# Optimization experiments

Hardware: AMD Instinct MI355X
Metric: run time of the kernel (lower is better)

## Reference

```python
import jax, jax.numpy as jnp
import numpy as np

B = 262144
D = 128          # d_model
DFF = 4 * D      # 512, FFN expansion
T = 16           # num_tiles
TPC = 4          # tiles_per_cluster
NC = T // TPC    # 4 clusters
NOPS = 8         # len(OPCODES)
EMB = 32
FEAT = EMB + 17  # 49
TW, SW, DW = 0.01, 0.005, 0.01  # ternary / sparsity / diversity weights


def ternary_quant(W):
    # per-tile ternary quantization: threshold at 0.7 * mean|W|, scale = mean|W|
    s0 = jnp.mean(jnp.abs(W))
    return s0 * jnp.sign(W) * (jnp.abs(W) > 0.7 * s0).astype(W.dtype)


def setup_inputs() -> dict:
    key = jax.random.key(0)
    ks = jax.random.split(key, 16)
    inp = {
        'op_idx': jax.random.randint(ks[0], (B,), 0, NOPS),
        'a': jax.random.randint(ks[1], (B,), 0, 256),
        'b': jax.random.randint(ks[2], (B,), 0, 256),
        'c': jax.random.randint(ks[3], (B,), 0, 2),
        # parameters
        'op_embed': jax.random.normal(ks[4], (NOPS, EMB), jnp.float32),
        'W_in': jax.random.normal(ks[5], (FEAT, D), jnp.float32) / np.sqrt(FEAT),
        'b_in': jnp.zeros((D,), jnp.float32),
        'Wr': jax.random.normal(ks[6], (D, T), jnp.float32) / np.sqrt(D),
        'W1': jax.random.normal(ks[7], (T, D, DFF), jnp.float32) / np.sqrt(D),
        'W2': jax.random.normal(ks[8], (T, DFF, D), jnp.float32) / np.sqrt(DFF),
        'Wh1': jax.random.normal(ks[9], (D, 64), jnp.float32) / np.sqrt(D),
        'bh1': jnp.zeros((64,), jnp.float32),
        'Wh2': jax.random.normal(ks[10], (64, 8), jnp.float32) / np.sqrt(64),
        'bh2': jnp.zeros((8,), jnp.float32),
    }
    return inp


def reference(op_embed, W_in, b_in, Wr, W1, W2, Wh1, bh1, Wh2, bh2, op_idx, a, b, c):
    bits = lambda v: ((v[:, None] >> jnp.arange(8)) & 1).astype(jnp.float32)  # [B,8]
    emb = op_embed[op_idx]  # [B,32]
    x = jnp.concatenate([emb, bits(a), bits(b), c[:, None].astype(jnp.float32)], axis=1)  # [B,49]
    x = x @ W_in + b_in  # [B,D]

    # tile routing (top-1)
    logits = x @ Wr                      # [B,T]
    probs = jax.nn.softmax(logits, -1)
    idx = jnp.argmax(probs, -1)          # [B]
    gate = jnp.max(probs, -1)            # [B]

    # ternary-quantized per-tile FFN weights
    W1q = jax.vmap(ternary_quant)(W1)    # [T,D,DFF]
    W2q = jax.vmap(ternary_quant)(W2)    # [T,DFF,D]

    out = jnp.zeros_like(x)
    for t in range(T):  # fixed small tile set
        y = jax.nn.gelu(x @ W1q[t]) @ W2q[t]          # [B,D]
        out = out + jnp.where((idx == t)[:, None], y, 0.0)
    out = out * gate[:, None]

    # aux losses
    one_hot = jax.nn.one_hot(idx, T, dtype=x.dtype)
    frac = one_hot.mean(0)               # tokens per tile
    meanp = probs.mean(0)                # mean router prob per tile
    sparsity = T * jnp.sum(frac * meanp)              # load-balance (Switch-style)
    tern = jnp.mean(jnp.abs(W1 - W1q)) + jnp.mean(jnp.abs(W2 - W2q))
    cp = meanp.reshape(NC, TPC).sum(-1)               # cluster usage
    diversity = jnp.sum(cp * jnp.log(cp + 1e-9))      # negative entropy
    aux = TW * tern + SW * sparsity + DW * diversity

    h = jax.nn.relu(out @ Wh1 + bh1)
    result = jax.nn.sigmoid(h @ Wh2 + bh2)  # [B,8]
    return result, idx, aux
```

## Files before the change

### kernel.cpp

```cpp
#include <hip/hip_runtime.h>
#include <hip/hip_bf16.h>
#include <math.h>

typedef __attribute__((ext_vector_type(8))) short short8;
typedef __attribute__((ext_vector_type(4))) float floatx4;
typedef __attribute__((ext_vector_type(4))) unsigned int uintx4;
typedef __attribute__((ext_vector_type(2))) unsigned int uintx2;

__device__ __forceinline__ unsigned short f2bf(float f) {
    unsigned int u = __float_as_uint(f);
    unsigned int r = (u + 0x7fffu + ((u >> 16) & 1u)) >> 16;
    return (unsigned short)r;
}

__device__ __forceinline__ unsigned int cvtpk(float a, float b) {
    unsigned int r;
    asm("v_cvt_pk_bf16_f32 %0, %1, %2" : "=v"(r) : "v"(a), "v"(b));
    return r;
}

__device__ __forceinline__ void permlane32_swap(unsigned int &a, unsigned int &b) {
    asm volatile("v_permlane32_swap_b32 %0, %1" : "+v"(a), "+v"(b));
}
__device__ __forceinline__ void permlane16_swap(unsigned int &a, unsigned int &b) {
    asm volatile("v_permlane16_swap_b32 %0, %1" : "+v"(a), "+v"(b));
}

__device__ __forceinline__ float gelu_f(float u) {
    float u2 = u * u;
    float p = __builtin_fmaf(u2, -0.102943242f, -2.302208184f);
    float z = p * u;
    float e;
    asm("v_exp_f32 %0, %1" : "=v"(e) : "v"(z));
    return u * __builtin_amdgcn_rcpf(1.0f + e);
}

__device__ __forceinline__ floatx4 mfma16(short8 a, short8 b, floatx4 c) {
    return __builtin_amdgcn_mfma_f32_16x16x32_bf16(a, b, c, 0, 0, 0);
}


__global__ __launch_bounds__(256) void k_prep1(
        const float* __restrict__ W1, const float* __restrict__ W2,
        float* __restrict__ partials,
        const float* __restrict__ op_embed, const float* __restrict__ W_in,
        const float* __restrict__ b_in,
        float* embW, float* Ta, float* Tb, float* Tc) {
    __shared__ float red[256];
    int bid = blockIdx.x;
    if (bid < 512) {
        bool isW1 = bid < 256;
        const float* W = (isW1 ? W1 : W2) + (long)(isW1 ? bid : bid - 256) * 4096;
        float s = 0.f;
        #pragma unroll
        for (int i = 0; i < 4; i++) {
            floatx4 v = *(const floatx4*)(W + i * 1024 + threadIdx.x * 4);
            s += fabsf(v[0]) + fabsf(v[1]) + fabsf(v[2]) + fabsf(v[3]);
        }
        red[threadIdx.x] = s; __syncthreads();
        for (int st = 128; st > 0; st >>= 1) {
            if (threadIdx.x < st) red[threadIdx.x] += red[threadIdx.x + st];
            __syncthreads();
        }
        if (threadIdx.x == 0) partials[bid] = red[0];
    } else {
        int i = (bid - 512) * 256 + threadIdx.x;
        if (i < 1024) {
            int op = i >> 7, j = i & 127;
            float s = b_in[j];
            #pragma unroll
            for (int k = 0; k < 32; k++) s += op_embed[op * 32 + k] * W_in[k * 128 + j];
            embW[i] = s;
        } else if (i < 1024 + 32768) {
            int r = i - 1024; int a = r >> 7, j = r & 127;
            float s = 0.f;
            #pragma unroll
            for (int bit = 0; bit < 8; bit++) if ((a >> bit) & 1) s += W_in[(32 + bit) * 128 + j];
            Ta[r] = s;
        } else if (i < 33792 + 32768) {
            int r = i - 33792; int b = r >> 7, j = r & 127;
            float s = 0.f;
            #pragma unroll
            for (int bit = 0; bit < 8; bit++) if ((b >> bit) & 1) s += W_in[(40 + bit) * 128 + j];
            Tb[r] = s;
        } else if (i < 66560 + 128) {
            int j = i - 66560; Tc[j] = W_in[48 * 128 + j];
        }
    }
}


__global__ __launch_bounds__(256) void k_prep2(
        const float* __restrict__ W1, const float* __restrict__ W2,
        const float* __restrict__ partials,
        unsigned short* __restrict__ W1qT, unsigned short* __restrict__ W2qT,
        float* ternsum,
        const float* __restrict__ embW, const float* __restrict__ Ta,
        const float* __restrict__ Tb, const float* __restrict__ Tc,
        const float* __restrict__ Wr,
        float* embWr, float* TaR, float* TbR, float* TcR) {
    __shared__ unsigned short Lq[4096];
    __shared__ float red[256];
    int blk = blockIdx.x;
    if (blk >= 512) {
        int i = (blk - 512) * 256 + threadIdx.x;
        int row = i >> 4, t = i & 15;
        const float* src; float* dst;
        if (row < 8)        { src = embW + row * 128;        dst = embWr + i; }
        else if (row < 264) { src = Ta + (row - 8) * 128;    dst = TaR + (row - 8) * 16 + t; }
        else if (row < 520) { src = Tb + (row - 264) * 128;  dst = TbR + (row - 264) * 16 + t; }
        else if (row == 520){ src = Tc;                      dst = TcR + t; }
        else return;
        float s = 0.f;
        for (int j = 0; j < 128; j++) s += src[j] * Wr[j * 16 + t];
        *dst = s;
        return;
    }
    bool isW1 = blk < 256;
    int rb = isW1 ? blk : blk - 256;
    int t = rb >> 4, slab = rb & 15;
    const float* part = partials + (isW1 ? 0 : 256) + t * 16;
    float ssum = 0.f;
    #pragma unroll
    for (int i = 0; i < 16; i++) ssum += part[i];
    float s = ssum * (1.0f / 65536.0f);
    float thr = 0.7f * s;
    unsigned int us = (unsigned int)f2bf(s);
    int tid = threadIdx.x;
    float dsum = 0.f;
    if (isW1) {
        int f0 = slab * 32;
        int d = tid >> 1, fh = (tid & 1) * 16;
        const float* src = W1 + (long)t * 65536 + d * 512 + f0 + fh;
        #pragma unroll
        for (int i = 0; i < 4; i++) {
            floatx4 w = *(const floatx4*)(src + i * 4);
            #pragma unroll
            for (int r = 0; r < 4; r++) {
                float wv = w[r];
                float aw = fabsf(wv);
                bool big = aw > thr;
                dsum += big ? fabsf(aw - s) : aw;
                unsigned int sign15 = (__float_as_uint(wv) >> 16) & 0x8000u;
                unsigned short q = big ? (unsigned short)(us | sign15) : (unsigned short)0;
                Lq[(fh + i * 4 + r) * 128 + d] = q;
            }
        }
    } else {
        int d0 = slab * 8;
        int f = tid * 2;
        const float* src = W2 + (long)t * 65536 + f * 128 + d0;
        #pragma unroll
        for (int rr = 0; rr < 2; rr++) {
            #pragma unroll
            for (int i = 0; i < 2; i++) {
                floatx4 w = *(const floatx4*)(src + rr * 128 + i * 4);
                #pragma unroll
                for (int r = 0; r < 4; r++) {
                    float wv = w[r];
                    float aw = fabsf(wv);
                    bool big = aw > thr;
                    dsum += big ? fabsf(aw - s) : aw;
                    unsigned int sign15 = (__float_as_uint(wv) >> 16) & 0x8000u;
                    unsigned short q = big ? (unsigned short)(us | sign15) : (unsigned short)0;
                    Lq[(i * 4 + r) * 512 + f + rr] = q;
                }
            }
        }
    }
    __syncthreads();
    unsigned short* dst = (isW1 ? W1qT : W2qT) + (long)t * 65536 + slab * 4096;
    const uintx4* Ls = (const uintx4*)Lq;
    uintx4* D4 = (uintx4*)dst;
    D4[tid] = Ls[tid];
    D4[tid + 256] = Ls[tid + 256];
    red[tid] = dsum; __syncthreads();
    for (int st2 = 128; st2 > 0; st2 >>= 1) {
        if (tid < st2) red[tid] += red[tid + st2];
        __syncthreads();
    }
    if (tid == 0) atomicAdd(ternsum, red[0]);
}


__global__ __launch_bounds__(256) void k_main3(
        const int* __restrict__ op_idx, const int* __restrict__ a_in,
        const int* __restrict__ b_in_i, const int* __restrict__ c_in,
        const float* __restrict__ embW, const float* __restrict__ Ta,
        const float* __restrict__ Tb, const float* __restrict__ Tc,
        const float* __restrict__ embWr, const float* __restrict__ TaR,
        const float* __restrict__ TbR, const float* __restrict__ TcR,
        unsigned short* __restrict__ xq, float* __restrict__ gate_out,
        float* psum, int* cnt, float* __restrict__ d_idx,
        const unsigned short* __restrict__ W2qT, const float* __restrict__ Wh1,
        unsigned short* __restrict__ W23qT) {
    __shared__ float sp[4][16];
    __shared__ int sc[4][16];
    __shared__ float wcol[128];

    if (blockIdx.x >= 1024) {
        int b2 = blockIdx.x - 1024;
        int t = b2 >> 6, h = b2 & 63;
        if (threadIdx.x < 128) wcol[threadIdx.x] = Wh1[threadIdx.x * 64 + h];
        __syncthreads();
        int k2 = threadIdx.x * 2;
        const unsigned short* w2 = W2qT + (long)t * 65536 + k2;
        float a0 = 0.f, a1 = 0.f;
        #pragma unroll 8
        for (int d = 0; d < 128; d++) {
            unsigned int u = *(const unsigned int*)(w2 + d * 512);
            float w = wcol[d];
            a0 += w * __uint_as_float(u << 16);
            a1 += w * __uint_as_float(u & 0xffff0000u);
        }
        *(unsigned int*)(W23qT + ((long)(t * 64 + h)) * 512 + k2) = cvtpk(a0, a1);
        return;
    }

    int gid = blockIdx.x * 256 + threadIdx.x;
    int lane = threadIdx.x & 63;
    int j = lane & 15;
    int grpbase = lane & 48;
    float psum_acc = 0.f; int cnt_acc = 0;

    #pragma unroll 1
    for (int it = 0; it < 16; it++) {
        int tok = it * 16384 + (gid >> 4);
        int op = op_idx[tok], a = a_in[tok], b = b_in_i[tok], c = c_in[tok];
        float cf = (float)c;

        float lg = embWr[op * 16 + j] + TaR[a * 16 + j] + TbR[b * 16 + j] + cf * TcR[j];
        float m = lg;
        m = fmaxf(m, __shfl_xor(m, 8, 16));
        m = fmaxf(m, __shfl_xor(m, 4, 16));
        m = fmaxf(m, __shfl_xor(m, 2, 16));
        m = fmaxf(m, __shfl_xor(m, 1, 16));
        float p = __expf(lg - m);
        float s = p;
        s += __shfl_xor(s, 8, 16);
        s += __shfl_xor(s, 4, 16);
        s += __shfl_xor(s, 2, 16);
        s += __shfl_xor(s, 1, 16);
        float g = __builtin_amdgcn_rcpf(s);
        unsigned long long ball = __ballot(lg == m);
        int bi = __ffsll((unsigned long long)((ball >> grpbase) & 0xffffULL)) - 1;
        psum_acc += p * g;
        cnt_acc += (j == bi) ? 1 : 0;
        if (j == 0) { gate_out[tok] = g; d_idx[tok] = (float)bi; }

        int d0 = j * 8;
        const floatx4* E  = (const floatx4*)(embW + op * 128 + d0);
        const floatx4* A4 = (const floatx4*)(Ta + a * 128 + d0);
        const floatx4* B4 = (const floatx4*)(Tb + b * 128 + d0);
        const floatx4* C4 = (const floatx4*)(Tc + d0);
        floatx4 v0 = E[0] + A4[0] + B4[0] + cf * C4[0];
        floatx4 v1 = E[1] + A4[1] + B4[1] + cf * C4[1];
        uintx4 o;
        o[0] = cvtpk(v0[0], v0[1]);
        o[1] = cvtpk(v0[2], v0[3]);
        o[2] = cvtpk(v1[0], v1[1]);
        o[3] = cvtpk(v1[2], v1[3]);
        *(uintx4*)(xq + (long)tok * 128 + d0) = o;
    }

    psum_acc += __shfl_xor(psum_acc, 16);
    psum_acc += __shfl_xor(psum_acc, 32);
    cnt_acc += __shfl_xor(cnt_acc, 16);
    cnt_acc += __shfl_xor(cnt_acc, 32);
    int wv = threadIdx.x >> 6;
    if (lane < 16) { sp[wv][j] = psum_acc; sc[wv][j] = cnt_acc; }
    __syncthreads();
    if (threadIdx.x < 16) {
        int jj = threadIdx.x;
        atomicAdd(&psum[jj], sp[0][jj] + sp[1][jj] + sp[2][jj] + sp[3][jj]);
        atomicAdd(&cnt[jj], sc[0][jj] + sc[1][jj] + sc[2][jj] + sc[3][jj]);
    }
}


__global__ void k_scatter(const float* __restrict__ d_idx, const int* __restrict__ cnt,
                          int* fill, int* __restrict__ bucket) {
    __shared__ int lc[16], lbase[16];
    if (threadIdx.x < 16) lc[threadIdx.x] = 0;
    __syncthreads();
    int offs[16];
    {
        int off = 0;
        #pragma unroll
        for (int tt = 0; tt < 16; tt++) { offs[tt] = off; off += cnt[tt]; }
    }
    int tok = blockIdx.x * 256 + threadIdx.x;
    int t = (int)d_idx[tok];
    int lpos = atomicAdd(&lc[t], 1);
    __syncthreads();
    if (threadIdx.x < 16) lbase[threadIdx.x] = atomicAdd(&fill[threadIdx.x], lc[threadIdx.x]);
    __syncthreads();
    bucket[offs[t] + lbase[t] + lpos] = tok;
}


__global__ __launch_bounds__(256, 3) void k_ffn(
    const unsigned short* __restrict__ xq, const float* __restrict__ gate,
    const int* __restrict__ bucket, const int* __restrict__ cnt_g,
    const float* __restrict__ psum_g, const float* __restrict__ ternsum_g,
    const unsigned short* __restrict__ W1qT, const unsigned short* __restrict__ W23qT,
    const float* __restrict__ Wh2, const float* __restrict__ bh1,
    const float* __restrict__ bh2,
    float* __restrict__ result, float* __restrict__ d_aux) {

    extern __shared__ __align__(16) unsigned char smem[];
    unsigned short* Ax = (unsigned short*)smem;
    float* Red = (float*)(smem + 17408);
    int*   toks = (int*)(smem + 33792);
    float* gats = (float*)(smem + 34048);
    float* Wh2l = (float*)(smem + 34304);
    float* bh2l = (float*)(smem + 36352);
    float* bh1l = (float*)(smem + 36384);

    int bid = blockIdx.x;
    int t = -1, ci = 0, nt = 0, base = 0;
    {
        int coff = 0, off = 0;
        #pragma unroll 1
        for (int tt = 0; tt < 16; tt++) {
            int c = cnt_g[tt];
            int ch = (c + 63) >> 6;
            if (t < 0 && bid < coff + ch) { t = tt; ci = bid - coff; nt = c; base = off + ci * 64; }
            coff += ch; off += c;
        }
    }
    if (t < 0) return;
    int nvalid = nt - ci * 64; if (nvalid > 64) nvalid = 64;

    int tid = threadIdx.x;
    if (tid < 64) {
        int tk = (tid < nvalid) ? bucket[base + tid] : -1;
        toks[tid] = tk;
        gats[tid] = (tk >= 0) ? gate[tk] : 0.0f;
    }
    Wh2l[tid] = Wh2[tid];
    Wh2l[tid + 256] = Wh2[tid + 256];
    if (tid < 8) bh2l[tid] = bh2[tid];
    else if (tid < 72) bh1l[tid - 8] = bh1[tid - 8];
    __syncthreads();

    #pragma unroll
    for (int it = 0; it < 4; it++) {
        int seg = it * 256 + tid; int r = seg >> 4, sg = seg & 15;
        int tk = toks[r];
        uintx4 v = {0u, 0u, 0u, 0u};
        if (tk >= 0) v = *(const uintx4*)(xq + (long)tk * 128 + sg * 8);
        *(uintx4*)(Ax + r * 136 + sg * 8) = v;
    }
    __syncthreads();

    int lane = tid & 63, dh = tid >> 6;
    int lane15 = lane & 15, lgrp = lane >> 4;

    floatx4 acc3[4][4];
    #pragma unroll
    for (int i = 0; i < 4; i++)
        #pragma unroll
        for (int j = 0; j < 4; j++) acc3[i][j] = (floatx4){0.f, 0.f, 0.f, 0.f};

    const unsigned short* w1p  = W1qT + (long)t * 65536 + (dh * 32 + lane15) * 128 + lgrp * 8;
    const unsigned short* w23p = W23qT + (long)t * 32768 + lane15 * 512 + dh * 32 + lgrp * 8;
    int ho0 = dh * 8192;
    int ho1 = ((dh + 1) & 3) * 8192;
    int ho2 = ((dh + 2) & 3) * 8192;
    int ho3 = ((dh + 3) & 3) * 8192;

    for (int nc = 0; nc < 4; nc++) {
        floatx4 acc1[2][4];
        #pragma unroll
        for (int i = 0; i < 2; i++)
            #pragma unroll
            for (int j = 0; j < 4; j++) acc1[i][j] = (floatx4){0.f, 0.f, 0.f, 0.f};

        const unsigned short* w1c = w1p + nc * 16384;
        #pragma unroll
        for (int kk = 0; kk < 4; kk++) {
            short8 af0 = *(const short8*)(w1c + kk * 32);
            short8 af1 = *(const short8*)(w1c + 2048 + kk * 32);
            int ko = kk * 32 + lgrp * 8;
            #pragma unroll
            for (int mt = 0; mt < 4; mt++) {
                short8 bf = *(const short8*)(Ax + (mt * 16 + lane15) * 136 + ko);
                acc1[0][mt] = mfma16(af0, bf, acc1[0][mt]);
                acc1[1][mt] = mfma16(af1, bf, acc1[1][mt]);
            }
        }

        const unsigned short* w23c = w23p + nc * 128;
        short8 af23_0 = *(const short8*)(w23c + ho0);
        short8 af23_1 = *(const short8*)(w23c + ho1);
        short8 af23_2 = *(const short8*)(w23c + ho2);
        short8 af23_3 = *(const short8*)(w23c + ho3);

        #pragma unroll
        for (int mt = 0; mt < 4; mt++) {
            floatx4 v0 = acc1[0][mt], v1 = acc1[1][mt];
            unsigned int X0 = cvtpk(gelu_f(v0[0]), gelu_f(v0[1]));
            unsigned int X1 = cvtpk(gelu_f(v0[2]), gelu_f(v0[3]));
            unsigned int Y0 = cvtpk(gelu_f(v1[0]), gelu_f(v1[1]));
            unsigned int Y1 = cvtpk(gelu_f(v1[2]), gelu_f(v1[3]));
            permlane32_swap(X0, Y0);
            permlane16_swap(X0, Y0);
            permlane32_swap(X1, Y1);
            permlane16_swap(X1, Y1);
            union { uintx4 u; short8 s; } bu;
            bu.u[0] = X0; bu.u[1] = X1; bu.u[2] = Y0; bu.u[3] = Y1;
            short8 bfrag = bu.s;
            acc3[0][mt] = mfma16(af23_0, bfrag, acc3[0][mt]);
            acc3[1][mt] = mfma16(af23_1, bfrag, acc3[1][mt]);
            acc3[2][mt] = mfma16(af23_2, bfrag, acc3[2][mt]);
            acc3[3][mt] = mfma16(af23_3, bfrag, acc3[3][mt]);
        }
    }

    floatx4 fin[4];
    #pragma unroll
    for (int mt = 0; mt < 4; mt++) fin[mt] = acc3[0][mt];
    float* myslot = Red + dh * 1024;
    int lofs = lane * 4;
    #pragma unroll
    for (int mt = 0; mt < 4; mt++)
        *(floatx4*)(myslot + mt * 256 + lofs) = acc3[1][mt];
    __syncthreads();
    {
        const float* ps = Red + ((dh + 3) & 3) * 1024;
        #pragma unroll
        for (int mt = 0; mt < 4; mt++)
            fin[mt] += *(const floatx4*)(ps + mt * 256 + lofs);
    }
    __syncthreads();
    #pragma unroll
    for (int mt = 0; mt < 4; mt++)
        *(floatx4*)(myslot + mt * 256 + lofs) = acc3[2][mt];
    __syncthreads();
    {
        const float* ps = Red + ((dh + 2) & 3) * 1024;
        #pragma unroll
        for (int mt = 0; mt < 4; mt++)
            fin[mt] += *(const floatx4*)(ps + mt * 256 + lofs);
    }
    __syncthreads();
    #pragma unroll
    for (int mt = 0; mt < 4; mt++)
        *(floatx4*)(myslot + mt * 256 + lofs) = acc3[3][mt];
    __syncthreads();
    {
        const float* ps = Red + ((dh + 1) & 3) * 1024;
        #pragma unroll
        for (int mt = 0; mt < 4; mt++)
            fin[mt] += *(const floatx4*)(ps + mt * 256 + lofs);
    }

    float* H = (float*)Ax;
    int hb = dh * 16 + lgrp * 4;
    floatx4 b4 = *(const floatx4*)(bh1l + hb);
    #pragma unroll
    for (int mt = 0; mt < 4; mt++) {
        int m = mt * 16 + lane15;
        float gm = gats[m];
        floatx4 v;
        v[0] = fmaxf(fin[mt][0] * gm + b4[0], 0.f);
        v[1] = fmaxf(fin[mt][1] * gm + b4[1], 0.f);
        v[2] = fmaxf(fin[mt][2] * gm + b4[2], 0.f);
        v[3] = fmaxf(fin[mt][3] * gm + b4[3], 0.f);
        *(floatx4*)(H + m * 68 + hb) = v;
    }
    __syncthreads();

    int mloc = tid >> 2, c0 = (tid & 3) * 2;
    int tk = toks[mloc];
    float z0 = bh2l[c0], z1 = bh2l[c0 + 1];
    const floatx4* Hr4 = (const floatx4*)(H + mloc * 68);
    #pragma unroll
    for (int h4 = 0; h4 < 16; h4++) {
        floatx4 hv = Hr4[h4];
        #pragma unroll
        for (int r = 0; r < 4; r++) {
            int h = h4 * 4 + r;
            z0 += hv[r] * Wh2l[h * 8 + c0];
            z1 += hv[r] * Wh2l[h * 8 + c0 + 1];
        }
    }
    if (tk >= 0) {
        float2 rr;
        rr.x = __builtin_amdgcn_rcpf(1.0f + __expf(-z0));
        rr.y = __builtin_amdgcn_rcpf(1.0f + __expf(-z1));
        *(float2*)(result + (long)tk * 8 + c0) = rr;
    }

    if (bid == 0 && tid == 0) {
        const float Bf = 262144.0f;
        float tern = ternsum_g[0] * (1.0f / 1048576.0f);
        float sp = 0.f; float cp[4] = {0.f, 0.f, 0.f, 0.f};
        for (int tt = 0; tt < 16; tt++) {
            float frac = (float)cnt_g[tt] / Bf, mp = psum_g[tt] / Bf;
            sp += frac * mp; cp[tt >> 2] += mp;
        }
        float dv = 0.f;
        for (int cc = 0; cc < 4; cc++) dv += cp[cc] * logf(cp[cc] + 1e-9f);
        d_aux[0] = 0.01f * tern + 0.005f * (16.0f * sp) + 0.01f * dv;
    }
}


extern "C" void kernel_launch(void* const* d_in, const int* in_sizes, int n_in,
                              void* d_out, int out_size, void* d_ws, size_t ws_size,
                              hipStream_t stream) {
    const int* op_idx = (const int*)d_in[0];
    const int* a_in   = (const int*)d_in[1];
    const int* b_in_i = (const int*)d_in[2];
    const int* c_in   = (const int*)d_in[3];
    const float* op_embed = (const float*)d_in[4];
    const float* W_in  = (const float*)d_in[5];
    const float* b_in  = (const float*)d_in[6];
    const float* Wr    = (const float*)d_in[7];
    const float* W1    = (const float*)d_in[8];
    const float* W2    = (const float*)d_in[9];
    const float* Wh1   = (const float*)d_in[10];
    const float* bh1   = (const float*)d_in[11];
    const float* Wh2   = (const float*)d_in[12];
    const float* bh2   = (const float*)d_in[13];

    const long B = in_sizes[0];
    float* result = (float*)d_out;
    float* d_idx  = (float*)d_out + B * 8;
    float* d_aux  = (float*)d_out + B * 9;

    unsigned char* ws = (unsigned char*)d_ws;
    unsigned short* xq    = (unsigned short*)(ws + 0);
    unsigned short* W1qT  = (unsigned short*)(ws + 67108864);
    unsigned short* W2qT  = (unsigned short*)(ws + 69206016);
    unsigned short* W23qT = (unsigned short*)(ws + 71303168);
    float* gate  = (float*)(ws + 72351744);
    int*   bucket= (int*)  (ws + 73400320);
    float* Ta    = (float*)(ws + 74448896);
    float* Tb    = (float*)(ws + 74579968);
    float* embW  = (float*)(ws + 74711040);
    float* Tc    = (float*)(ws + 74715136);
    float* TaR   = (float*)(ws + 74715648);
    float* TbR   = (float*)(ws + 74732032);
    float* embWr = (float*)(ws + 74748416);
    float* TcR   = (float*)(ws + 74748928);
    float* partials = (float*)(ws + 74748992);
    unsigned char* acc = ws + 74751040;
    float* ternsum = (float*)(acc + 0);
    float* psum    = (float*)(acc + 64);
    int*   cnt     = (int*)(acc + 128);
    int*   fill    = (int*)(acc + 192);

    hipMemsetAsync(acc, 0, 256, stream);

    k_prep1<<<773, 256, 0, stream>>>(W1, W2, partials, op_embed, W_in, b_in,
                                     embW, Ta, Tb, Tc);
    k_prep2<<<545, 256, 0, stream>>>(W1, W2, partials, W1qT, W2qT, ternsum,
                                     embW, Ta, Tb, Tc, Wr, embWr, TaR, TbR, TcR);
    k_main3<<<2048, 256, 0, stream>>>(op_idx, a_in, b_in_i, c_in,
                                      embW, Ta, Tb, Tc, embWr, TaR, TbR, TcR,
                                      xq, gate, psum, cnt, d_idx,
                                      W2qT, Wh1, W23qT);
    k_scatter<<<(int)(B / 256), 256, 0, stream>>>(d_idx, cnt, fill, bucket);
    k_ffn<<<4112, 256, 36640, stream>>>(xq, gate, bucket, cnt, psum, ternsum,
                                        W1qT, W23qT, Wh2, bh1, bh2, result, d_aux);
}
```

Measured before the change: 266.6 us.

## Recompute input embeddings inside FFN kernel instead of materializing xq

Removes the bf16 xq activation buffer written by the routing kernel and read back by the FFN kernel. The FFN kernel now gathers op/a/b/c per token and rebuilds each row from the small precomputed embedding tables. This drops roughly 64MB of write plus read traffic in exchange for extra table gathers and index loads inside the FFN kernel. It also reorders the first GEMM loop so all W1 fragments are loaded up front and the nc loop is fully unrolled, which raises register pressure.

```diff
diff --git a/kernel.cpp b/kernel.cpp
--- a/kernel.cpp
+++ b/kernel.cpp
@@ -5,7 +5,6 @@
 typedef __attribute__((ext_vector_type(8))) short short8;
 typedef __attribute__((ext_vector_type(4))) float floatx4;
 typedef __attribute__((ext_vector_type(4))) unsigned int uintx4;
-typedef __attribute__((ext_vector_type(2))) unsigned int uintx2;
 
 __device__ __forceinline__ unsigned short f2bf(float f) {
     unsigned int u = __float_as_uint(f);
@@ -186,11 +185,9 @@
 __global__ __launch_bounds__(256) void k_main3(
         const int* __restrict__ op_idx, const int* __restrict__ a_in,
         const int* __restrict__ b_in_i, const int* __restrict__ c_in,
-        const float* __restrict__ embW, const float* __restrict__ Ta,
-        const float* __restrict__ Tb, const float* __restrict__ Tc,
         const float* __restrict__ embWr, const float* __restrict__ TaR,
         const float* __restrict__ TbR, const float* __restrict__ TcR,
-        unsigned short* __restrict__ xq, float* __restrict__ gate_out,
+        float* __restrict__ gate_out,
         float* psum, int* cnt, float* __restrict__ d_idx,
         const unsigned short* __restrict__ W2qT, const float* __restrict__ Wh1,
         unsigned short* __restrict__ W23qT) {
@@ -247,20 +244,6 @@
         psum_acc += p * g;
         cnt_acc += (j == bi) ? 1 : 0;
         if (j == 0) { gate_out[tok] = g; d_idx[tok] = (float)bi; }
-
-        int d0 = j * 8;
-        const floatx4* E  = (const floatx4*)(embW + op * 128 + d0);
-        const floatx4* A4 = (const floatx4*)(Ta + a * 128 + d0);
-        const floatx4* B4 = (const floatx4*)(Tb + b * 128 + d0);
-        const floatx4* C4 = (const floatx4*)(Tc + d0);
-        floatx4 v0 = E[0] + A4[0] + B4[0] + cf * C4[0];
-        floatx4 v1 = E[1] + A4[1] + B4[1] + cf * C4[1];
-        uintx4 o;
-        o[0] = cvtpk(v0[0], v0[1]);
-        o[1] = cvtpk(v0[2], v0[3]);
-        o[2] = cvtpk(v1[0], v1[1]);
-        o[3] = cvtpk(v1[2], v1[3]);
-        *(uintx4*)(xq + (long)tok * 128 + d0) = o;
     }
 
     psum_acc += __shfl_xor(psum_acc, 16);
@@ -300,7 +283,11 @@
 
 
 __global__ __launch_bounds__(256, 3) void k_ffn(
-    const unsigned short* __restrict__ xq, const float* __restrict__ gate,
+    const int* __restrict__ op_idx, const int* __restrict__ a_in,
+    const int* __restrict__ b_in_i, const int* __restrict__ c_in,
+    const float* __restrict__ embW, const float* __restrict__ Ta,
+    const float* __restrict__ Tb, const float* __restrict__ Tc,
+    const float* __restrict__ gate,
     const int* __restrict__ bucket, const int* __restrict__ cnt_g,
     const float* __restrict__ psum_g, const float* __restrict__ ternsum_g,
     const unsigned short* __restrict__ W1qT, const unsigned short* __restrict__ W23qT,
@@ -316,6 +303,10 @@
     float* Wh2l = (float*)(smem + 34304);
     float* bh2l = (float*)(smem + 36352);
     float* bh1l = (float*)(smem + 36384);
+    int*   opsl = (int*)(smem + 36640);
+    int*   asl  = (int*)(smem + 36896);
+    int*   bsl  = (int*)(smem + 37152);
+    float* csl  = (float*)(smem + 37408);
 
     int bid = blockIdx.x;
     int t = -1, ci = 0, nt = 0, base = 0;
@@ -336,7 +327,12 @@
     if (tid < 64) {
         int tk = (tid < nvalid) ? bucket[base + tid] : -1;
         toks[tid] = tk;
+        int tks = (tk >= 0) ? tk : 0;
         gats[tid] = (tk >= 0) ? gate[tk] : 0.0f;
+        opsl[tid] = op_idx[tks];
+        asl[tid]  = a_in[tks];
+        bsl[tid]  = b_in_i[tks];
+        csl[tid]  = (float)c_in[tks];
     }
     Wh2l[tid] = Wh2[tid];
     Wh2l[tid + 256] = Wh2[tid + 256];
@@ -347,10 +343,21 @@
     #pragma unroll
     for (int it = 0; it < 4; it++) {
         int seg = it * 256 + tid; int r = seg >> 4, sg = seg & 15;
-        int tk = toks[r];
-        uintx4 v = {0u, 0u, 0u, 0u};
-        if (tk >= 0) v = *(const uintx4*)(xq + (long)tk * 128 + sg * 8);
-        *(uintx4*)(Ax + r * 136 + sg * 8) = v;
+        int d0 = sg * 8;
+        int op = opsl[r], a = asl[r], b = bsl[r];
+        float cf = csl[r];
+        const floatx4* Ev = (const floatx4*)(embW + op * 128 + d0);
+        const floatx4* A4 = (const floatx4*)(Ta + a * 128 + d0);
+        const floatx4* B4 = (const floatx4*)(Tb + b * 128 + d0);
+        const floatx4* C4 = (const floatx4*)(Tc + d0);
+        floatx4 v0 = Ev[0] + A4[0] + B4[0] + cf * C4[0];
+        floatx4 v1 = Ev[1] + A4[1] + B4[1] + cf * C4[1];
+        uintx4 o;
+        o[0] = cvtpk(v0[0], v0[1]);
+        o[1] = cvtpk(v0[2], v0[3]);
+        o[2] = cvtpk(v1[0], v1[1]);
+        o[3] = cvtpk(v1[2], v1[3]);
+        *(uintx4*)(Ax + r * 136 + sg * 8) = o;
     }
     __syncthreads();
 
@@ -370,32 +377,46 @@
     int ho2 = ((dh + 2) & 3) * 8192;
     int ho3 = ((dh + 3) & 3) * 8192;
 
+    #pragma unroll
     for (int nc = 0; nc < 4; nc++) {
-        floatx4 acc1[2][4];
-        #pragma unroll
-        for (int i = 0; i < 2; i++)
-            #pragma unroll
-            for (int j = 0; j < 4; j++) acc1[i][j] = (floatx4){0.f, 0.f, 0.f, 0.f};
-
         const unsigned short* w1c = w1p + nc * 16384;
-        #pragma unroll
-        for (int kk = 0; kk < 4; kk++) {
-            short8 af0 = *(const short8*)(w1c + kk * 32);
-            short8 af1 = *(const short8*)(w1c + 2048 + kk * 32);
-            int ko = kk * 32 + lgrp * 8;
-            #pragma unroll
-            for (int mt = 0; mt < 4; mt++) {
-                short8 bf = *(const short8*)(Ax + (mt * 16 + lane15) * 136 + ko);
-                acc1[0][mt] = mfma16(af0, bf, acc1[0][mt]);
-                acc1[1][mt] = mfma16(af1, bf, acc1[1][mt]);
-            }
-        }
-
         const unsigned short* w23c = w23p + nc * 128;
+
+        short8 a00 = *(const short8*)(w1c + 0 * 32);
+        short8 a01 = *(const short8*)(w1c + 1 * 32);
+        short8 a02 = *(const short8*)(w1c + 2 * 32);
+        short8 a03 = *(const short8*)(w1c + 3 * 32);
+        short8 a10 = *(const short8*)(w1c + 2048 + 0 * 32);
+        short8 a11 = *(const short8*)(w1c + 2048 + 1 * 32);
+        short8 a12 = *(const short8*)(w1c + 2048 + 2 * 32);
+        short8 a13 = *(const short8*)(w1c + 2048 + 3 * 32);
         short8 af23_0 = *(const short8*)(w23c + ho0);
         short8 af23_1 = *(const short8*)(w23c + ho1);
         short8 af23_2 = *(const short8*)(w23c + ho2);
         short8 af23_3 = *(const short8*)(w23c + ho3);
+
+        floatx4 acc1[2][4];
+        #pragma unroll
+        for (int i = 0; i < 2; i++)
+            #pragma unroll
+            for (int j = 0; j < 4; j++) acc1[i][j] = (floatx4){0.f, 0.f, 0.f, 0.f};
+
+        #pragma unroll
+        for (int mt = 0; mt < 4; mt++) {
+            int mrow = (mt * 16 + lane15) * 136;
+            short8 bf0 = *(const short8*)(Ax + mrow + 0 * 32 + lgrp * 8);
+            short8 bf1 = *(const short8*)(Ax + mrow + 1 * 32 + lgrp * 8);
+            short8 bf2 = *(const short8*)(Ax + mrow + 2 * 32 + lgrp * 8);
+            short8 bf3 = *(const short8*)(Ax + mrow + 3 * 32 + lgrp * 8);
+            acc1[0][mt] = mfma16(a00, bf0, acc1[0][mt]);
+            acc1[1][mt] = mfma16(a10, bf0, acc1[1][mt]);
+            acc1[0][mt] = mfma16(a01, bf1, acc1[0][mt]);
+            acc1[1][mt] = mfma16(a11, bf1, acc1[1][mt]);
+            acc1[0][mt] = mfma16(a02, bf2, acc1[0][mt]);
+            acc1[1][mt] = mfma16(a12, bf2, acc1[1][mt]);
+            acc1[0][mt] = mfma16(a03, bf3, acc1[0][mt]);
+            acc1[1][mt] = mfma16(a13, bf3, acc1[1][mt]);
+        }
 
         #pragma unroll
         for (int mt = 0; mt < 4; mt++) {
@@ -532,7 +553,6 @@
     float* d_aux  = (float*)d_out + B * 9;
 
     unsigned char* ws = (unsigned char*)d_ws;
-    unsigned short* xq    = (unsigned short*)(ws + 0);
     unsigned short* W1qT  = (unsigned short*)(ws + 67108864);
     unsigned short* W2qT  = (unsigned short*)(ws + 69206016);
     unsigned short* W23qT = (unsigned short*)(ws + 71303168);
@@ -560,10 +580,12 @@
     k_prep2<<<545, 256, 0, stream>>>(W1, W2, partials, W1qT, W2qT, ternsum,
                                      embW, Ta, Tb, Tc, Wr, embWr, TaR, TbR, TcR);
     k_main3<<<2048, 256, 0, stream>>>(op_idx, a_in, b_in_i, c_in,
-                                      embW, Ta, Tb, Tc, embWr, TaR, TbR, TcR,
-                                      xq, gate, psum, cnt, d_idx,
+                                      embWr, TaR, TbR, TcR,
+                                      gate, psum, cnt, d_idx,
                                       W2qT, Wh1, W23qT);
     k_scatter<<<(int)(B / 256), 256, 0, stream>>>(d_idx, cnt, fill, bucket);
-    k_ffn<<<4112, 256, 36640, stream>>>(xq, gate, bucket, cnt, psum, ternsum,
+    k_ffn<<<4112, 256, 37664, stream>>>(op_idx, a_in, b_in_i, c_in,
+                                        embW, Ta, Tb, Tc,
+                                        gate, bucket, cnt, psum, ternsum,
                                         W1qT, W23qT, Wh2, bh1, bh2, result, d_aux);
 }
```

Result: no change. 264.4 us (-0.8%).
